# Kernel tuning notes

Measured on AMD Instinct MI355X. Metric: run time of the kernel, lower is better.

## Reference

```python
import jax, jax.numpy as jnp
import numpy as np

EMBED_DIM = 1024
NUM_HEADS = 16
HEAD_DIM = EMBED_DIM // NUM_HEADS


def setup_inputs() -> dict:
    key = jax.random.key(0)
    k1, k2, k3, k4, k5 = jax.random.split(key, 5)
    s = 1.0 / np.sqrt(EMBED_DIM)
    return {
        "query": jax.random.normal(k1, (8, 1024, EMBED_DIM), dtype=jnp.float32),
        "w_qkv": jax.random.normal(k2, (EMBED_DIM, 3 * EMBED_DIM), dtype=jnp.float32) * s,
        "b_qkv": jax.random.normal(k3, (3 * EMBED_DIM,), dtype=jnp.float32) * 0.01,
        "w_proj": jax.random.normal(k4, (EMBED_DIM, EMBED_DIM), dtype=jnp.float32) * s,
        "b_proj": jax.random.normal(k5, (EMBED_DIM,), dtype=jnp.float32) * 0.01,
    }


def reference(query, w_qkv, b_qkv, w_proj, b_proj):
    B, S, D = query.shape
    H, Hd = NUM_HEADS, HEAD_DIM
    scale = 1.0 / jnp.sqrt(jnp.asarray(Hd, query.dtype))
    # fused QKV projection; key=value=query (self-attention), so one GEMM suffices
    qkv = query @ w_qkv + b_qkv                      # [B, S, 3D]
    qkv = qkv.reshape(B, S, 3, H, Hd)
    q = qkv[:, :, 0].transpose(0, 2, 1, 3)           # [B, H, S, Hd]
    k = qkv[:, :, 1].transpose(0, 2, 1, 3)
    v = qkv[:, :, 2].transpose(0, 2, 1, 3)
    attn = jnp.einsum("bhqd,bhkd->bhqk", q, k) * scale
    attn = jax.nn.softmax(attn, axis=-1)
    out = jnp.einsum("bhqk,bhkd->bhqd", attn, v)     # [B, H, S, Hd]
    out = out.transpose(0, 2, 1, 3).reshape(B, S, D)
    return out @ w_proj + b_proj
```

## Files before the change

kernel.cpp:

```cpp
#include <hip/hip_runtime.h>
#include <stdint.h>

#define DEV __device__ __forceinline__

typedef short bf16x8 __attribute__((ext_vector_type(8)));
typedef float f32x4 __attribute__((ext_vector_type(4)));
typedef float f32x16 __attribute__((ext_vector_type(16)));
typedef unsigned u32x2 __attribute__((ext_vector_type(2)));

DEV short f2bf(float f) {
  uint32_t x = __builtin_bit_cast(uint32_t, f);
  uint32_t r = x + 0x7fffu + ((x >> 16) & 1u);
  return (short)(r >> 16);
}

DEV unsigned cvtpk(float lo, float hi) {
  unsigned r;
  asm("v_cvt_pk_bf16_f32 %0, %1, %2" : "=v"(r) : "v"(lo), "v"(hi));
  return r;
}
DEV void pswap(unsigned& a, unsigned& b) {
  asm("v_permlane32_swap_b32 %0, %1" : "+v"(a), "+v"(b));
}

DEV void gld16(const short* g, short* l) {
  __builtin_amdgcn_global_load_lds(
      (const __attribute__((address_space(1))) void*)g,
      (__attribute__((address_space(3))) void*)l, 16, 0, 0);
}

__global__ __launch_bounds__(256) void k_cvt(const float* __restrict__ in,
                                             short* __restrict__ out, int n8) {
  int i = blockIdx.x * 256 + threadIdx.x;
  if (i >= n8) return;
  const float4* p = (const float4*)in + (size_t)i * 2;
  float4 a = p[0], b = p[1];
  bf16x8 v;
  v[0] = f2bf(a.x); v[1] = f2bf(a.y); v[2] = f2bf(a.z); v[3] = f2bf(a.w);
  v[4] = f2bf(b.x); v[5] = f2bf(b.y); v[6] = f2bf(b.z); v[7] = f2bf(b.w);
  *(bf16x8*)(out + (size_t)i * 8) = v;
}

__global__ __launch_bounds__(256) void k_tcvt(const float* __restrict__ in,
                                              short* __restrict__ out, int K, int N) {
  __shared__ float tile[64][65];
  int t = threadIdx.x;
  int n0 = blockIdx.x * 64, k0 = blockIdx.y * 64;
  int kl = t >> 4, nl = (t & 15) * 4;
#pragma unroll
  for (int it = 0; it < 4; ++it) {
    float4 v = *(const float4*)&in[(size_t)(k0 + kl + it * 16) * N + n0 + nl];
    tile[nl + 0][kl + it * 16] = v.x;
    tile[nl + 1][kl + it * 16] = v.y;
    tile[nl + 2][kl + it * 16] = v.z;
    tile[nl + 3][kl + it * 16] = v.w;
  }
  __syncthreads();
  int no = t >> 2, kc = (t & 3) * 16;
  bf16x8 v0, v1;
#pragma unroll
  for (int c = 0; c < 8; ++c) v0[c] = f2bf(tile[no][kc + c]);
#pragma unroll
  for (int c = 0; c < 8; ++c) v1[c] = f2bf(tile[no][kc + 8 + c]);
  size_t ob = (size_t)(n0 + no) * K + k0 + kc;
  *(bf16x8*)&out[ob] = v0;
  *(bf16x8*)&out[ob + 8] = v1;
}

__global__ __launch_bounds__(256) void k_vt(const short* __restrict__ vin,
                                            short* __restrict__ vt) {
  __shared__ alignas(16) short tile[64][72];
  int t = threadIdx.x;
  int sc = blockIdx.x, bh = blockIdx.y;
  int sl = t >> 3, dc = (t & 7) * 8;
  const short* base = vin + ((size_t)bh * 1024 + sc * 64) * 64;
#pragma unroll
  for (int it = 0; it < 2; ++it)
    *(bf16x8*)&tile[sl + it * 32][dc] = *(const bf16x8*)&base[(size_t)(sl + it * 32) * 64 + dc];
  __syncthreads();
  int d = t >> 2, s2 = (t & 3) * 16;
  bf16x8 v0, v1;
#pragma unroll
  for (int c = 0; c < 8; ++c) v0[c] = tile[s2 + c][d];
#pragma unroll
  for (int c = 0; c < 8; ++c) v1[c] = tile[s2 + 8 + c][d];
  size_t ob = (size_t)bh * 65536 + (size_t)d * 1024 + sc * 64 + s2;
  *(bf16x8*)&vt[ob] = v0;
  *(bf16x8*)&vt[ob + 8] = v1;
}

template <int MODE>
__global__ __launch_bounds__(256) void k_gemm(const short* __restrict__ A,
                                              const short* __restrict__ Bw,
                                              const float* __restrict__ bias,
                                              void* o0, void* o1, void* o2) {
  __shared__ alignas(16) short lA[2][128 * 64];
  __shared__ alignas(16) short lB[2][128 * 64];
  int t = threadIdx.x;
  int w = t >> 6, l = t & 63;
  int wr = w >> 1, wc = w & 1;
  int lr = l & 15, lg = l >> 4;
  int m0 = blockIdx.y * 128, n0 = blockIdx.x * 128;
  f32x4 acc[4][4] = {};

  int srow = t >> 3;
  int schunk = (t & 7) ^ (srow & 7);
  const short* ap = A + (size_t)(m0 + srow) * 1024 + schunk * 8;
  const short* bp = Bw + (size_t)(n0 + srow) * 1024 + schunk * 8;
  int lofs = w * 8 * 64;

#define GSTAGE(buf, k0)                                                  \
  do {                                                                   \
    short* la0 = &lA[buf][lofs];                                         \
    short* lb0 = &lB[buf][lofs];                                         \
    _Pragma("unroll")                                                    \
    for (int c = 0; c < 4; ++c) {                                        \
      gld16(ap + (size_t)c * 32 * 1024 + (k0), la0 + c * 32 * 64);       \
      gld16(bp + (size_t)c * 32 * 1024 + (k0), lb0 + c * 32 * 64);       \
    }                                                                    \
  } while (0)

  GSTAGE(0, 0);
  for (int it = 0; it < 16; ++it) {
    int p = it & 1;
    if (it < 15) {
      GSTAGE(p ^ 1, (it + 1) * 64);
      asm volatile("s_waitcnt vmcnt(8)" ::: "memory");
    } else {
      asm volatile("s_waitcnt vmcnt(0)" ::: "memory");
    }
    __builtin_amdgcn_sched_barrier(0);
    __builtin_amdgcn_s_barrier();
    __builtin_amdgcn_sched_barrier(0);

    bf16x8 af[4][2], bfr[4][2];
#pragma unroll
    for (int i = 0; i < 4; ++i)
#pragma unroll
      for (int kh = 0; kh < 2; ++kh) {
        int ra = wr * 64 + i * 16 + lr;
        int rb = wc * 64 + i * 16 + lr;
        af[i][kh] = *(const bf16x8*)&lA[p][ra * 64 + (((kh * 4 + lg) ^ (ra & 7)) * 8)];
        bfr[i][kh] = *(const bf16x8*)&lB[p][rb * 64 + (((kh * 4 + lg) ^ (rb & 7)) * 8)];
      }
    __builtin_amdgcn_s_setprio(1);
#pragma unroll
    for (int i = 0; i < 4; ++i)
#pragma unroll
      for (int j = 0; j < 4; ++j)
#pragma unroll
        for (int kh = 0; kh < 2; ++kh)
          acc[i][j] = __builtin_amdgcn_mfma_f32_16x16x32_bf16(af[i][kh], bfr[j][kh], acc[i][j], 0, 0, 0);
    __builtin_amdgcn_s_setprio(0);

    __builtin_amdgcn_sched_barrier(0);
    __builtin_amdgcn_s_barrier();
    __builtin_amdgcn_sched_barrier(0);
  }
#undef GSTAGE

  if (MODE == 0) {
    short* outs[3] = {(short*)o0, (short*)o1, (short*)o2};
    short* op = outs[n0 >> 10];
    float qs = (n0 < 1024) ? 0.18033688011112042f : 1.0f;
#pragma unroll
    for (int i = 0; i < 4; ++i)
#pragma unroll
      for (int j = 0; j < 4; ++j)
#pragma unroll
        for (int r = 0; r < 4; ++r) {
          int mm = m0 + wr * 64 + i * 16 + lg * 4 + r;
          int nn = n0 + wc * 64 + j * 16 + lr;
          float val = (acc[i][j][r] + bias[nn]) * qs;
          int hh = (nn >> 6) & 15, dd = nn & 63;
          int bb = mm >> 10, ss = mm & 1023;
          op[((size_t)(bb * 16 + hh) * 1024 + ss) * 64 + dd] = f2bf(val);
        }
  } else {
    float* op = (float*)o0;
#pragma unroll
    for (int i = 0; i < 4; ++i)
#pragma unroll
      for (int j = 0; j < 4; ++j)
#pragma unroll
        for (int r = 0; r < 4; ++r) {
          int mm = m0 + wr * 64 + i * 16 + lg * 4 + r;
          int nn = n0 + wc * 64 + j * 16 + lr;
          op[(size_t)mm * 1024 + nn] = acc[i][j][r] + bias[nn];
        }
  }
}

__global__ __launch_bounds__(256, 4) void k_attn(const short* __restrict__ qb,
                                                 const short* __restrict__ kb,
                                                 const short* __restrict__ vt,
                                                 short* __restrict__ ao) {
  __shared__ alignas(16) short lds[2 * 8192];
  int t = threadIdx.x, w = t >> 6, l = t & 63;
  int r0 = l & 31, hi = l >> 5;

  int bid = blockIdx.x;
  int swz = (bid & 7) * 128 + (bid >> 3);
  int bh = swz >> 3, qc = swz & 7;
  int q0 = qc * 128 + w * 32;

  const short* qbase = qb + (size_t)bh * 65536;
  const short* kbase = kb + (size_t)bh * 65536;
  const short* vbase = vt + (size_t)bh * 65536;

  bf16x8 qf[4];
#pragma unroll
  for (int step = 0; step < 4; ++step)
    qf[step] = *(const bf16x8*)&qbase[(size_t)(q0 + r0) * 64 + step * 16 + hi * 8];

  f32x16 acc0 = {0,0,0,0,0,0,0,0,0,0,0,0,0,0,0,0};
  f32x16 acc1 = {0,0,0,0,0,0,0,0,0,0,0,0,0,0,0,0};
  float ls = 0.f;

  int srow = t >> 3;
  int sch = (t & 7) ^ (srow & 7);
  const short* kp = kbase + (size_t)srow * 64 + sch * 8;
  const short* vp = vbase + (size_t)srow * 1024 + sch * 8;

#define STAGE(buf, kv0)                                              \
  do {                                                               \
    short* dk = &lds[(buf) * 8192 + w * 512];                        \
    short* dv = &lds[(buf) * 8192 + 4096 + w * 512];                 \
    gld16(kp + (size_t)(kv0) * 64, dk);                              \
    gld16(kp + (size_t)((kv0) + 32) * 64, dk + 2048);                \
    gld16(vp + (kv0), dv);                                           \
    gld16(vp + (kv0) + 32 * 1024, dv + 2048);                        \
  } while (0)

  STAGE(0, 0);
  int cur = 0;
  for (int it = 0; it < 16; ++it) {
    __syncthreads();
    if (it < 15) STAGE(cur ^ 1, (it + 1) * 64);
    const short* lk = &lds[cur * 8192];
    const short* lv = &lds[cur * 8192 + 4096];

    f32x16 s0 = {0,0,0,0,0,0,0,0,0,0,0,0,0,0,0,0};
    f32x16 s1 = {0,0,0,0,0,0,0,0,0,0,0,0,0,0,0,0};
    __builtin_amdgcn_s_setprio(1);
#pragma unroll
    for (int step = 0; step < 4; ++step) {
      int ck = step * 2 + hi;
      bf16x8 kf0 = *(const bf16x8*)&lk[r0 * 64 + ((ck ^ (r0 & 7)) * 8)];
      int r1 = 32 + r0;
      bf16x8 kf1 = *(const bf16x8*)&lk[r1 * 64 + ((ck ^ (r1 & 7)) * 8)];
      s0 = __builtin_amdgcn_mfma_f32_32x32x16_bf16(kf0, qf[step], s0, 0, 0, 0);
      s1 = __builtin_amdgcn_mfma_f32_32x32x16_bf16(kf1, qf[step], s1, 0, 0, 0);
    }
    __builtin_amdgcn_s_setprio(0);

    float rs = 0.f;
#pragma unroll
    for (int r = 0; r < 16; ++r) { float p = __builtin_exp2f(s0[r]); s0[r] = p; rs += p; }
#pragma unroll
    for (int r = 0; r < 16; ++r) { float p = __builtin_exp2f(s1[r]); s1[r] = p; rs += p; }
    rs += __shfl_xor(rs, 32);
    ls += rs;

    __builtin_amdgcn_s_setprio(1);
#pragma unroll
    for (int tt = 0; tt < 2; ++tt) {
#pragma unroll
      for (int ks = 0; ks < 2; ++ks) {
        unsigned Aw, Bw2, Cw, Dw;
        if (tt == 0) {
          Aw = cvtpk(s0[8 * ks + 0], s0[8 * ks + 1]);
          Bw2 = cvtpk(s0[8 * ks + 4], s0[8 * ks + 5]);
          Cw = cvtpk(s0[8 * ks + 2], s0[8 * ks + 3]);
          Dw = cvtpk(s0[8 * ks + 6], s0[8 * ks + 7]);
        } else {
          Aw = cvtpk(s1[8 * ks + 0], s1[8 * ks + 1]);
          Bw2 = cvtpk(s1[8 * ks + 4], s1[8 * ks + 5]);
          Cw = cvtpk(s1[8 * ks + 2], s1[8 * ks + 3]);
          Dw = cvtpk(s1[8 * ks + 6], s1[8 * ks + 7]);
        }
        pswap(Aw, Bw2);
        pswap(Cw, Dw);
        union { unsigned u[4]; bf16x8 v; } pb;
        pb.u[0] = Aw; pb.u[1] = Cw; pb.u[2] = Bw2; pb.u[3] = Dw;
        int cv = tt * 4 + ks * 2 + hi;
        bf16x8 vf0 = *(const bf16x8*)&lv[r0 * 64 + ((cv ^ (r0 & 7)) * 8)];
        int r1 = 32 + r0;
        bf16x8 vf1 = *(const bf16x8*)&lv[r1 * 64 + ((cv ^ (r1 & 7)) * 8)];
        acc0 = __builtin_amdgcn_mfma_f32_32x32x16_bf16(vf0, pb.v, acc0, 0, 0, 0);
        acc1 = __builtin_amdgcn_mfma_f32_32x32x16_bf16(vf1, pb.v, acc1, 0, 0, 0);
      }
    }
    __builtin_amdgcn_s_setprio(0);
    cur ^= 1;
  }
#undef STAGE

  __syncthreads();
  short* ep = &lds[w * 2048];
  float inv = 1.0f / ls;
#pragma unroll
  for (int d0 = 0; d0 < 2; ++d0) {
#pragma unroll
    for (int q4 = 0; q4 < 4; ++q4) {
      unsigned w0, w1;
      if (d0 == 0) {
        w0 = cvtpk(acc0[q4 * 4 + 0] * inv, acc0[q4 * 4 + 1] * inv);
        w1 = cvtpk(acc0[q4 * 4 + 2] * inv, acc0[q4 * 4 + 3] * inv);
      } else {
        w0 = cvtpk(acc1[q4 * 4 + 0] * inv, acc1[q4 * 4 + 1] * inv);
        w1 = cvtpk(acc1[q4 * 4 + 2] * inv, acc1[q4 * 4 + 3] * inv);
      }
      int chunk = (q4 + 4 * d0) ^ (r0 & 7);
      u32x2 uv; uv[0] = w0; uv[1] = w1;
      *(u32x2*)((char*)ep + r0 * 128 + chunk * 16 + hi * 8) = uv;
    }
  }
  int b = bh >> 4, hh = bh & 15;
#pragma unroll
  for (int rr = 0; rr < 4; ++rr) {
    int row = (l >> 3) + rr * 8;
    int c = (l & 7) ^ (row & 7);
    bf16x8 ov = *(const bf16x8*)((char*)ep + row * 128 + c * 16);
    int tok = b * 1024 + q0 + row;
    *(bf16x8*)&ao[(size_t)tok * 1024 + hh * 64 + (l & 7) * 8] = ov;
  }
}

extern "C" void kernel_launch(void* const* d_in, const int* in_sizes, int n_in,
                              void* d_out, int out_size, void* d_ws, size_t ws_size,
                              hipStream_t stream) {
  const float* query  = (const float*)d_in[0];
  const float* w_qkv  = (const float*)d_in[1];
  const float* b_qkv  = (const float*)d_in[2];
  const float* w_proj = (const float*)d_in[3];
  const float* b_proj = (const float*)d_in[4];
  float* out = (float*)d_out;
  char* ws = (char*)d_ws;

  short* qbf = (short*)(ws);
  short* wT  = (short*)(ws + 16777216);
  short* wpT = (short*)(ws + 23068672);
  short* qb  = (short*)(ws + 25165824);
  short* kb  = (short*)(ws + 41943040);
  short* vb  = (short*)(ws + 58720256);
  short* vt  = (short*)(ws + 75497472);
  short* ao  = qbf;

  k_cvt<<<4096, 256, 0, stream>>>(query, qbf, 1048576);
  k_tcvt<<<dim3(48, 16), 256, 0, stream>>>(w_qkv, wT, 1024, 3072);
  k_tcvt<<<dim3(16, 16), 256, 0, stream>>>(w_proj, wpT, 1024, 1024);
  k_gemm<0><<<dim3(24, 64), 256, 0, stream>>>(qbf, wT, b_qkv, qb, kb, vb);
  k_vt<<<dim3(16, 128), 256, 0, stream>>>(vb, vt);
  k_attn<<<1024, 256, 0, stream>>>(qb, kb, vt, ao);
  k_gemm<1><<<dim3(8, 64), 256, 0, stream>>>(ao, wpT, b_proj, out, nullptr, nullptr);
}
```

Baseline: 183.3 us.

## Enlarge GEMM tiles to 256x128 with 8 waves and split-phase loads

The GEMM kernel now uses 512-thread blocks covering 256x128 output tiles, so each B tile loaded from global memory serves twice as many rows. Each k-step is split into two half-phases: B fragments and half of the A fragments are read, their MFMAs run, then the other half of A is read while the second half of the next stage's global loads is issued. This aims to cut global traffic per output and to overlap loads with compute better. In exchange, LDS use rises to 96KB per block with fewer blocks per CU, more barriers per iteration, and grid sizes of 768 and 256 blocks that may leave the CUs unevenly loaded.

```diff
diff --git a/kernel.cpp b/kernel.cpp
--- a/kernel.cpp
+++ b/kernel.cpp
@@ -90,88 +90,117 @@
 }
 
 template <int MODE>
-__global__ __launch_bounds__(256) void k_gemm(const short* __restrict__ A,
-                                              const short* __restrict__ Bw,
-                                              const float* __restrict__ bias,
-                                              void* o0, void* o1, void* o2) {
-  __shared__ alignas(16) short lA[2][128 * 64];
+__global__ __launch_bounds__(512, 2) void k_gemm(const short* __restrict__ A,
+                                                 const short* __restrict__ Bw,
+                                                 const float* __restrict__ bias,
+                                                 void* o0, void* o1, void* o2) {
+  __shared__ alignas(16) short lA[2][256 * 64];
   __shared__ alignas(16) short lB[2][128 * 64];
   int t = threadIdx.x;
   int w = t >> 6, l = t & 63;
   int wr = w >> 1, wc = w & 1;
   int lr = l & 15, lg = l >> 4;
-  int m0 = blockIdx.y * 128, n0 = blockIdx.x * 128;
+  int m0 = blockIdx.y * 256, n0 = blockIdx.x * 128;
   f32x4 acc[4][4] = {};
 
   int srow = t >> 3;
   int schunk = (t & 7) ^ (srow & 7);
   const short* ap = A + (size_t)(m0 + srow) * 1024 + schunk * 8;
   const short* bp = Bw + (size_t)(n0 + srow) * 1024 + schunk * 8;
-  int lofs = w * 8 * 64;
-
-#define GSTAGE(buf, k0)                                                  \
-  do {                                                                   \
-    short* la0 = &lA[buf][lofs];                                         \
-    short* lb0 = &lB[buf][lofs];                                         \
-    _Pragma("unroll")                                                    \
-    for (int c = 0; c < 4; ++c) {                                        \
-      gld16(ap + (size_t)c * 32 * 1024 + (k0), la0 + c * 32 * 64);       \
-      gld16(bp + (size_t)c * 32 * 1024 + (k0), lb0 + c * 32 * 64);       \
-    }                                                                    \
-  } while (0)
-
-  GSTAGE(0, 0);
-  for (int it = 0; it < 16; ++it) {
-    int p = it & 1;
-    if (it < 15) {
-      GSTAGE(p ^ 1, (it + 1) * 64);
-      asm volatile("s_waitcnt vmcnt(8)" ::: "memory");
+  int lofs = w * 512;
+
+#define STG_A(buf, kt, blk) \
+  gld16(ap + (size_t)(blk) * 64 * 1024 + (kt) * 64, &lA[buf][(blk) * 4096 + lofs])
+#define STG_B(buf, kt, blk) \
+  gld16(bp + (size_t)(blk) * 64 * 1024 + (kt) * 64, &lB[buf][(blk) * 4096 + lofs])
+
+  STG_A(0, 0, 0); STG_A(0, 0, 1); STG_A(0, 0, 2); STG_A(0, 0, 3);
+  STG_B(0, 0, 0); STG_B(0, 0, 1);
+
+  for (int kt = 0; kt < 16; ++kt) {
+    int b = kt & 1;
+    bf16x8 bfr[4][2], af[2][2];
+
+    if (kt < 15) {
+      STG_A(b ^ 1, kt + 1, 0); STG_A(b ^ 1, kt + 1, 1); STG_B(b ^ 1, kt + 1, 0);
+      asm volatile("s_waitcnt vmcnt(3)" ::: "memory");
     } else {
       asm volatile("s_waitcnt vmcnt(0)" ::: "memory");
     }
     __builtin_amdgcn_sched_barrier(0);
     __builtin_amdgcn_s_barrier();
     __builtin_amdgcn_sched_barrier(0);
-
-    bf16x8 af[4][2], bfr[4][2];
-#pragma unroll
-    for (int i = 0; i < 4; ++i)
-#pragma unroll
-      for (int kh = 0; kh < 2; ++kh) {
-        int ra = wr * 64 + i * 16 + lr;
-        int rb = wc * 64 + i * 16 + lr;
-        af[i][kh] = *(const bf16x8*)&lA[p][ra * 64 + (((kh * 4 + lg) ^ (ra & 7)) * 8)];
-        bfr[i][kh] = *(const bf16x8*)&lB[p][rb * 64 + (((kh * 4 + lg) ^ (rb & 7)) * 8)];
-      }
+#pragma unroll
+    for (int nj = 0; nj < 4; ++nj)
+#pragma unroll
+      for (int ks = 0; ks < 2; ++ks) {
+        int rb = wc * 64 + nj * 16 + lr;
+        bfr[nj][ks] = *(const bf16x8*)&lB[b][rb * 64 + (((ks * 4 + lg) ^ (rb & 7)) * 8)];
+      }
+#pragma unroll
+    for (int i2 = 0; i2 < 2; ++i2)
+#pragma unroll
+      for (int ks = 0; ks < 2; ++ks) {
+        int ra = wr * 64 + i2 * 16 + lr;
+        af[i2][ks] = *(const bf16x8*)&lA[b][ra * 64 + (((ks * 4 + lg) ^ (ra & 7)) * 8)];
+      }
+    asm volatile("s_waitcnt lgkmcnt(0)" ::: "memory");
+    __builtin_amdgcn_sched_barrier(0);
     __builtin_amdgcn_s_setprio(1);
 #pragma unroll
-    for (int i = 0; i < 4; ++i)
-#pragma unroll
-      for (int j = 0; j < 4; ++j)
-#pragma unroll
-        for (int kh = 0; kh < 2; ++kh)
-          acc[i][j] = __builtin_amdgcn_mfma_f32_16x16x32_bf16(af[i][kh], bfr[j][kh], acc[i][j], 0, 0, 0);
+    for (int i2 = 0; i2 < 2; ++i2)
+#pragma unroll
+      for (int nj = 0; nj < 4; ++nj)
+#pragma unroll
+        for (int ks = 0; ks < 2; ++ks)
+          acc[i2][nj] = __builtin_amdgcn_mfma_f32_16x16x32_bf16(af[i2][ks], bfr[nj][ks], acc[i2][nj], 0, 0, 0);
     __builtin_amdgcn_s_setprio(0);
-
     __builtin_amdgcn_sched_barrier(0);
     __builtin_amdgcn_s_barrier();
     __builtin_amdgcn_sched_barrier(0);
-  }
-#undef GSTAGE
+
+#pragma unroll
+    for (int i2 = 0; i2 < 2; ++i2)
+#pragma unroll
+      for (int ks = 0; ks < 2; ++ks) {
+        int ra = wr * 64 + (2 + i2) * 16 + lr;
+        af[i2][ks] = *(const bf16x8*)&lA[b][ra * 64 + (((ks * 4 + lg) ^ (ra & 7)) * 8)];
+      }
+    if (kt < 15) { STG_A(b ^ 1, kt + 1, 2); STG_A(b ^ 1, kt + 1, 3); STG_B(b ^ 1, kt + 1, 1); }
+    __builtin_amdgcn_sched_barrier(0);
+    __builtin_amdgcn_s_barrier();
+    __builtin_amdgcn_sched_barrier(0);
+    asm volatile("s_waitcnt lgkmcnt(0)" ::: "memory");
+    __builtin_amdgcn_sched_barrier(0);
+    __builtin_amdgcn_s_setprio(1);
+#pragma unroll
+    for (int i2 = 0; i2 < 2; ++i2)
+#pragma unroll
+      for (int nj = 0; nj < 4; ++nj)
+#pragma unroll
+        for (int ks = 0; ks < 2; ++ks)
+          acc[2 + i2][nj] = __builtin_amdgcn_mfma_f32_16x16x32_bf16(af[i2][ks], bfr[nj][ks], acc[2 + i2][nj], 0, 0, 0);
+    __builtin_amdgcn_s_setprio(0);
+    __builtin_amdgcn_sched_barrier(0);
+    __builtin_amdgcn_s_barrier();
+    __builtin_amdgcn_sched_barrier(0);
+  }
+#undef STG_A
+#undef STG_B
 
   if (MODE == 0) {
     short* outs[3] = {(short*)o0, (short*)o1, (short*)o2};
     short* op = outs[n0 >> 10];
     float qs = (n0 < 1024) ? 0.18033688011112042f : 1.0f;
 #pragma unroll
-    for (int i = 0; i < 4; ++i)
-#pragma unroll
-      for (int j = 0; j < 4; ++j)
+    for (int mi = 0; mi < 4; ++mi)
+#pragma unroll
+      for (int nj = 0; nj < 4; ++nj)
 #pragma unroll
         for (int r = 0; r < 4; ++r) {
-          int mm = m0 + wr * 64 + i * 16 + lg * 4 + r;
-          int nn = n0 + wc * 64 + j * 16 + lr;
-          float val = (acc[i][j][r] + bias[nn]) * qs;
+          int mm = m0 + wr * 64 + mi * 16 + lg * 4 + r;
+          int nn = n0 + wc * 64 + nj * 16 + lr;
+          float val = (acc[mi][nj][r] + bias[nn]) * qs;
           int hh = (nn >> 6) & 15, dd = nn & 63;
           int bb = mm >> 10, ss = mm & 1023;
           op[((size_t)(bb * 16 + hh) * 1024 + ss) * 64 + dd] = f2bf(val);
@@ -179,14 +208,14 @@
   } else {
     float* op = (float*)o0;
 #pragma unroll
-    for (int i = 0; i < 4; ++i)
-#pragma unroll
-      for (int j = 0; j < 4; ++j)
+    for (int mi = 0; mi < 4; ++mi)
+#pragma unroll
+      for (int nj = 0; nj < 4; ++nj)
 #pragma unroll
         for (int r = 0; r < 4; ++r) {
-          int mm = m0 + wr * 64 + i * 16 + lg * 4 + r;
-          int nn = n0 + wc * 64 + j * 16 + lr;
-          op[(size_t)mm * 1024 + nn] = acc[i][j][r] + bias[nn];
+          int mm = m0 + wr * 64 + mi * 16 + lg * 4 + r;
+          int nn = n0 + wc * 64 + nj * 16 + lr;
+          op[(size_t)mm * 1024 + nn] = acc[mi][nj][r] + bias[nn];
         }
   }
 }
@@ -350,8 +379,8 @@
   k_cvt<<<4096, 256, 0, stream>>>(query, qbf, 1048576);
   k_tcvt<<<dim3(48, 16), 256, 0, stream>>>(w_qkv, wT, 1024, 3072);
   k_tcvt<<<dim3(16, 16), 256, 0, stream>>>(w_proj, wpT, 1024, 1024);
-  k_gemm<0><<<dim3(24, 64), 256, 0, stream>>>(qbf, wT, b_qkv, qb, kb, vb);
+  k_gemm<0><<<dim3(24, 32), 512, 0, stream>>>(qbf, wT, b_qkv, qb, kb, vb);
   k_vt<<<dim3(16, 128), 256, 0, stream>>>(vb, vt);
   k_attn<<<1024, 256, 0, stream>>>(qb, kb, vt, ao);
-  k_gemm<1><<<dim3(8, 64), 256, 0, stream>>>(ao, wpT, b_proj, out, nullptr, nullptr);
-}
+  k_gemm<1><<<dim3(8, 32), 512, 0, stream>>>(ao, wpT, b_proj, out, nullptr, nullptr);
+}
```

Measured after the change: 193.6 us. 1.06x slower.
